# Performance work log

Measured on AMD Instinct MI355X. Metric: run time of the kernel, lower is better.

Reference implementation:

```python
import jax, jax.numpy as jnp
import numpy as np

H = 128

def _gine_conv(x, ei, ea, w1, b1, w2, b2):
    # GINEConv (eps=0): out = MLP(x + sum_{j->i} relu(x_j + e_ji))
    src, dst = ei[0], ei[1]
    m = jax.nn.relu(x[src] + ea)                      # [E, H]
    agg = jax.ops.segment_sum(m, dst, num_segments=x.shape[0])
    h = x + agg
    return jax.nn.relu(h @ w1 + b1) @ w2 + b2

def _bn(x, gamma, beta, eps=1e-5):
    # BatchNorm1d over node dim, batch statistics (training mode)
    mu = jnp.mean(x, axis=0)
    var = jnp.mean((x - mu) ** 2, axis=0)
    return gamma * (x - mu) * jax.lax.rsqrt(var + eps) + beta

def _scatter_mean(vals, ids, mask, n):
    w = mask.astype(vals.dtype)
    s = jax.ops.segment_sum(vals * w[:, None], ids, num_segments=n)
    c = jax.ops.segment_sum(w, ids, num_segments=n)
    return s / jnp.maximum(c, 1.0)[:, None]


def setup_inputs() -> dict:
    key = jax.random.key(0)
    ks = jax.random.split(key, 20)
    Nf, Nt, S, K = 320000, 100000, 20000, 16
    Ei, Eg = 1280000, 800000
    sc = 1.0 / np.sqrt(H)
    inp = {}
    inp["h_flat"] = jax.random.normal(ks[0], (Nf, H), jnp.float32)
    inp["intra_ei"] = jax.random.randint(ks[1], (2, Ei), 0, Nf, jnp.int32)
    inp["ea_flat"] = jax.random.normal(ks[2], (Ei, H), jnp.float32)
    inp["valid"] = jnp.ones((Nf,), jnp.bool_)
    inp["node_ids"] = jax.random.randint(ks[3], (Nf,), 0, Nt, jnp.int32)
    inp["N_total"] = Nt
    inp["edge_index"] = jax.random.randint(ks[4], (2, Eg), 0, Nt, jnp.int32)
    inp["edge_attr"] = jax.random.normal(ks[5], (Eg, H), jnp.float32)
    inp["sub_batch"] = jax.random.randint(ks[6], (Nf,), 0, S, jnp.int32)
    inp["S"] = S
    inp["k"] = K
    inp["root_flat_idx"] = jax.random.randint(ks[7], (S,), 0, Nf, jnp.int32)
    inp["is_root"] = jnp.zeros((Nf,), jnp.bool_)
    # parameters
    inp["local_w1"] = jax.random.normal(ks[8], (H, H), jnp.float32) * sc
    inp["local_b1"] = jnp.zeros((H,), jnp.float32)
    inp["local_w2"] = jax.random.normal(ks[9], (H, H), jnp.float32) * sc
    inp["local_b2"] = jnp.zeros((H,), jnp.float32)
    inp["local_gamma"] = jnp.ones((H,), jnp.float32)
    inp["local_beta"] = jnp.zeros((H,), jnp.float32)
    inp["global_w1"] = jax.random.normal(ks[10], (H, H), jnp.float32) * sc
    inp["global_b1"] = jnp.zeros((H,), jnp.float32)
    inp["global_w2"] = jax.random.normal(ks[11], (H, H), jnp.float32) * sc
    inp["global_b2"] = jnp.zeros((H,), jnp.float32)
    inp["global_gamma"] = jnp.ones((H,), jnp.float32)
    inp["global_beta"] = jnp.zeros((H,), jnp.float32)
    inp["skip_w"] = jax.random.normal(ks[12], (H, H), jnp.float32) * sc
    inp["skip_b"] = jnp.zeros((H,), jnp.float32)
    inp["vv_w"] = jax.random.normal(ks[13], (H, H), jnp.float32) * sc
    inp["vv_b"] = jnp.zeros((H,), jnp.float32)
    inp["kk_w"] = jax.random.normal(ks[14], (H, H), jnp.float32) * sc
    inp["kk_b"] = jnp.zeros((H,), jnp.float32)
    return inp


def reference(h_flat, intra_ei, ea_flat, valid, node_ids, N_total, edge_index, edge_attr,
              sub_batch, S, k, root_flat_idx, is_root,
              local_w1, local_b1, local_w2, local_b2, local_gamma, local_beta,
              global_w1, global_b1, global_w2, global_b2, global_gamma, global_beta,
              skip_w, skip_b, vv_w, vv_b, kk_w, kk_b):
    valid_f = valid.astype(h_flat.dtype)[:, None]
    clamped_ids = jnp.maximum(node_ids, 0)
    valid_mask = node_ids >= 0

    h_skip = (h_flat @ skip_w + skip_b) * valid_f

    h1 = _gine_conv(h_flat, intra_ei, ea_flat, local_w1, local_b1, local_w2, local_b2)
    h1 = _bn(h1, local_gamma, local_beta) * valid_f

    x_sum = _scatter_mean(h_flat, clamped_ids, valid_mask, N_total)   # [N_total, H]
    h2 = _gine_conv(x_sum, edge_index, edge_attr, global_w1, global_b1, global_w2, global_b2)
    h2 = _bn(h2, global_gamma, global_beta)[clamped_ids] * valid_f

    root_ids = node_ids[root_flat_idx]
    root_valid = root_ids >= 0
    x_vv_canonical = _scatter_mean(h_flat[root_flat_idx], jnp.maximum(root_ids, 0), root_valid, N_total)
    x_vv = (x_vv_canonical[clamped_ids] @ vv_w + vv_b) * valid_f

    x_kk = (h_flat[root_flat_idx[sub_batch]] @ kk_w + kk_b) * valid_f

    out = jax.nn.relu(h_skip + h1 + h2 + x_vv + x_kk)
    # dropout p=0.0 -> identity
    return out * valid_f
```

## Files before the change

kernel.cpp:

```cpp
#include <hip/hip_runtime.h>

#define H    128
#define HQ   32
#define TM   64
#define NT   100000
#define XS   136


typedef __attribute__((ext_vector_type(8))) short short8;
typedef __attribute__((ext_vector_type(4))) float f32x4;

static __host__ int cdiv(long a, long b) { return (int)((a + b - 1) / b); }
static __host__ char* alignp(char* p) {
    return (char*)(((uintptr_t)p + 255) & ~(uintptr_t)255);
}

__device__ inline unsigned short f2bf(float f) {
    unsigned u = __float_as_uint(f);
    unsigned r = u + 0x7FFFu + ((u >> 16) & 1u);
    return (unsigned short)(r >> 16);
}
__device__ inline float bf2f(unsigned short u) {
    return __uint_as_float((unsigned)u << 16);
}

__global__ __launch_bounds__(256) void k_cvt(
    const float* __restrict__ in, unsigned short* __restrict__ out, long n8)
{
    long i = (long)blockIdx.x * 256 + threadIdx.x;
    if (i >= n8) return;
    float4 a = ((const float4*)in)[2 * i];
    float4 b = ((const float4*)in)[2 * i + 1];
    ushort4 lo; lo.x = f2bf(a.x); lo.y = f2bf(a.y); lo.z = f2bf(a.z); lo.w = f2bf(a.w);
    ushort4 hi; hi.x = f2bf(b.x); hi.y = f2bf(b.y); hi.z = f2bf(b.z); hi.w = f2bf(b.w);
    ((ushort4*)out)[2 * i]     = lo;
    ((ushort4*)out)[2 * i + 1] = hi;
}

struct CsrJobs {
    const int* ids[4];
    int* cnt[4];
    int* rp[4];
    int* cur[4];
    int* eid[4];
    int  E[4];
    int  N[4];
    int  histBase[5];
    int  scanBase[5];
};

__global__ __launch_bounds__(256) void k_gather_rid(
    const int* __restrict__ node_ids, const int* __restrict__ rfi,
    int* __restrict__ rid, int S)
{
    int i = blockIdx.x * 256 + threadIdx.x;
    if (i >= S) return;
    int nid = node_ids[rfi[i]];
    rid[i] = nid > 0 ? nid : 0;
}

__global__ __launch_bounds__(256) void k_hist4(CsrJobs jb)
{
    int b = blockIdx.x, sg = 0;
    while (b >= jb.histBase[sg + 1]) ++sg;
    int e = (b - jb.histBase[sg]) * 256 + threadIdx.x;
    if (e < jb.E[sg]) atomicAdd(&jb.cnt[sg][jb.ids[sg][e]], 1);
}

__global__ __launch_bounds__(256) void k_scanA4(CsrJobs jb, int* __restrict__ parts)
{
    int b = blockIdx.x, sg = 0;
    while (b >= jb.scanBase[sg + 1]) ++sg;
    int lb = b - jb.scanBase[sg];
    const int* cnt = jb.cnt[sg];
    int* rowptr = jb.rp[sg];
    int N = jb.N[sg];
    int* partials = parts + sg * 256;

    __shared__ int lsum[256];
    int tid = threadIdx.x;
    int base = lb * 2048 + tid * 8;
    int v[8];
    int tsum = 0;
#pragma unroll
    for (int i = 0; i < 8; ++i) {
        int idx = base + i;
        int t = (idx < N) ? cnt[idx] : 0;
        v[i] = tsum;
        tsum += t;
    }
    lsum[tid] = tsum;
    __syncthreads();
    for (int off = 1; off < 256; off <<= 1) {
        int t = (tid >= off) ? lsum[tid - off] : 0;
        __syncthreads();
        lsum[tid] += t;
        __syncthreads();
    }
    int texcl = lsum[tid] - tsum;
#pragma unroll
    for (int i = 0; i < 8; ++i) {
        int idx = base + i;
        if (idx < N) rowptr[idx] = v[i] + texcl;
    }
    if (tid == 255) partials[lb] = lsum[255];
}

__global__ __launch_bounds__(256) void k_scanB4(CsrJobs jb, int* __restrict__ parts)
{
    int sg = blockIdx.x;
    int P = jb.scanBase[sg + 1] - jb.scanBase[sg];
    int* partials = parts + sg * 256;
    int* rowptr = jb.rp[sg];
    int N = jb.N[sg];

    __shared__ int lsum[256];
    int tid = threadIdx.x;
    int val = (tid < P) ? partials[tid] : 0;
    lsum[tid] = val;
    __syncthreads();
    for (int off = 1; off < 256; off <<= 1) {
        int t = (tid >= off) ? lsum[tid - off] : 0;
        __syncthreads();
        lsum[tid] += t;
        __syncthreads();
    }
    if (tid < P) partials[tid] = lsum[tid] - val;
    if (tid == 255) rowptr[N] = lsum[255];
}

__global__ __launch_bounds__(256) void k_scanC4(CsrJobs jb, const int* __restrict__ parts)
{
    int b = blockIdx.x, sg = 0;
    while (b >= jb.scanBase[sg + 1]) ++sg;
    int lb = b - jb.scanBase[sg];
    int off = parts[sg * 256 + lb];
    int N = jb.N[sg];
    int* rowptr = jb.rp[sg];
    int* cursor = jb.cur[sg];
    int base = lb * 2048;
    for (int i = threadIdx.x; i < 2048; i += 256) {
        int g = base + i;
        if (g < N) {
            int v = rowptr[g] + off;
            rowptr[g] = v;
            cursor[g] = v;
        }
    }
}

__global__ __launch_bounds__(256) void k_fillperm4(CsrJobs jb)
{
    int b = blockIdx.x, sg = 0;
    while (b >= jb.histBase[sg + 1]) ++sg;
    int e = (b - jb.histBase[sg]) * 256 + threadIdx.x;
    if (e < jb.E[sg]) {
        int pos = atomicAdd(&jb.cur[sg][jb.ids[sg][e]], 1);
        jb.eid[sg][pos] = e;
    }
}

__global__ __launch_bounds__(256) void k_csr_edge_agg(
    const unsigned short* __restrict__ X, const float* __restrict__ EA,
    const int* __restrict__ src, const int* __restrict__ eid,
    const int* __restrict__ rowptr, unsigned short* __restrict__ OUT, int N)
{
    int idx = blockIdx.x * 256 + threadIdx.x;
    int n = idx >> 5, l = idx & 31;
    if (n >= N) return;
    int beg = rowptr[n], end = rowptr[n + 1];
    float4 acc = {0.f, 0.f, 0.f, 0.f};
    int j = beg;
    for (; j + 2 <= end; j += 2) {
        int e0 = eid[j], e1 = eid[j + 1];
        int s0 = src[e0], s1 = src[e1];
        float4 a0 = ((const float4*)(EA + (size_t)e0 * H))[l];
        ushort4 h0 = ((const ushort4*)(X + (size_t)s0 * H))[l];
        float4 a1 = ((const float4*)(EA + (size_t)e1 * H))[l];
        ushort4 h1 = ((const ushort4*)(X + (size_t)s1 * H))[l];
        acc.x += fmaxf(bf2f(h0.x) + a0.x, 0.f) + fmaxf(bf2f(h1.x) + a1.x, 0.f);
        acc.y += fmaxf(bf2f(h0.y) + a0.y, 0.f) + fmaxf(bf2f(h1.y) + a1.y, 0.f);
        acc.z += fmaxf(bf2f(h0.z) + a0.z, 0.f) + fmaxf(bf2f(h1.z) + a1.z, 0.f);
        acc.w += fmaxf(bf2f(h0.w) + a0.w, 0.f) + fmaxf(bf2f(h1.w) + a1.w, 0.f);
    }
    if (j < end) {
        int e = eid[j];
        int s = src[e];
        float4 a = ((const float4*)(EA + (size_t)e * H))[l];
        ushort4 h = ((const ushort4*)(X + (size_t)s * H))[l];
        acc.x += fmaxf(bf2f(h.x) + a.x, 0.f);
        acc.y += fmaxf(bf2f(h.y) + a.y, 0.f);
        acc.z += fmaxf(bf2f(h.z) + a.z, 0.f);
        acc.w += fmaxf(bf2f(h.w) + a.w, 0.f);
    }
    ushort4 o;
    o.x = f2bf(acc.x); o.y = f2bf(acc.y); o.z = f2bf(acc.z); o.w = f2bf(acc.w);
    ((ushort4*)(OUT + (size_t)n * H))[l] = o;
}

__global__ __launch_bounds__(256) void k_csr_mean(
    const unsigned short* __restrict__ X, const int* __restrict__ eid,
    const int* __restrict__ rowmap,
    const int* __restrict__ rowptr, unsigned short* __restrict__ OUT, int N)
{
    int idx = blockIdx.x * 256 + threadIdx.x;
    int n = idx >> 5, l = idx & 31;
    if (n >= N) return;
    int beg = rowptr[n], end = rowptr[n + 1];
    float4 acc = {0.f, 0.f, 0.f, 0.f};
    int j = beg;
    for (; j + 2 <= end; j += 2) {
        int e0 = eid[j], e1 = eid[j + 1];
        int f0 = rowmap ? rowmap[e0] : e0;
        int f1 = rowmap ? rowmap[e1] : e1;
        ushort4 h0 = ((const ushort4*)(X + (size_t)f0 * H))[l];
        ushort4 h1 = ((const ushort4*)(X + (size_t)f1 * H))[l];
        acc.x += bf2f(h0.x) + bf2f(h1.x); acc.y += bf2f(h0.y) + bf2f(h1.y);
        acc.z += bf2f(h0.z) + bf2f(h1.z); acc.w += bf2f(h0.w) + bf2f(h1.w);
    }
    if (j < end) {
        int e = eid[j];
        int fi = rowmap ? rowmap[e] : e;
        ushort4 h = ((const ushort4*)(X + (size_t)fi * H))[l];
        acc.x += bf2f(h.x); acc.y += bf2f(h.y);
        acc.z += bf2f(h.z); acc.w += bf2f(h.w);
    }
    float inv = 1.0f / fmaxf((float)(end - beg), 1.0f);
    ushort4 o;
    o.x = f2bf(acc.x * inv); o.y = f2bf(acc.y * inv);
    o.z = f2bf(acc.z * inv); o.w = f2bf(acc.w * inv);
    ((ushort4*)(OUT + (size_t)n * H))[l] = o;
}

__device__ inline void stage_x_copy(
    unsigned short* sX, const unsigned short* X1, const int* gidx,
    int r0, int M, int tid)
{
    int r = tid >> 2, q = tid & 3;
    int row = r0 + r;
    unsigned short* dst = &sX[r * XS + q * 32];
    if (row < M) {
        int sr = gidx ? gidx[row] : row;
        const ushort4* xp = (const ushort4*)(X1 + (size_t)sr * H + q * 32);
#pragma unroll
        for (int i = 0; i < 8; ++i) *(ushort4*)(dst + i * 4) = xp[i];
    } else {
#pragma unroll
        for (int i = 0; i < 8; ++i) *(ushort4*)(dst + i * 4) = ushort4{0, 0, 0, 0};
    }
}

__device__ inline void stage_x_sum(
    unsigned short* sX, const unsigned short* X1, const unsigned short* X2,
    int r0, int M, int tid)
{
    int r = tid >> 2, q = tid & 3;
    int row = r0 + r;
    unsigned short* dst = &sX[r * XS + q * 32];
    if (row < M) {
        const ushort4* xp = (const ushort4*)(X1 + (size_t)row * H + q * 32);
        const ushort4* yp = (const ushort4*)(X2 + (size_t)row * H + q * 32);
#pragma unroll
        for (int i = 0; i < 8; ++i) {
            ushort4 a = xp[i], b = yp[i];
            ushort4 o;
            o.x = f2bf(bf2f(a.x) + bf2f(b.x));
            o.y = f2bf(bf2f(a.y) + bf2f(b.y));
            o.z = f2bf(bf2f(a.z) + bf2f(b.z));
            o.w = f2bf(bf2f(a.w) + bf2f(b.w));
            *(ushort4*)(dst + i * 4) = o;
        }
    } else {
#pragma unroll
        for (int i = 0; i < 8; ++i) *(ushort4*)(dst + i * 4) = ushort4{0, 0, 0, 0};
    }
}

__device__ inline void stage_wt(unsigned short* sWT, const float* W, int tid)
{
    for (int f = tid; f < H * HQ; f += 256) {
        int k = f >> 5, n4 = (f & 31) * 4;
        float4 v = ((const float4*)W)[f];
        sWT[(n4 + 0) * XS + k] = f2bf(v.x);
        sWT[(n4 + 1) * XS + k] = f2bf(v.y);
        sWT[(n4 + 2) * XS + k] = f2bf(v.z);
        sWT[(n4 + 3) * XS + k] = f2bf(v.w);
    }
}

__global__ __launch_bounds__(256) void k_gemm(
    const unsigned short* __restrict__ X1, const int* __restrict__ gidx,
    const float* __restrict__ W, const float* __restrict__ B,
    unsigned short* __restrict__ OUT, int M)
{
    __shared__ unsigned short sX[TM * XS];
    __shared__ unsigned short sWT[H * XS];
    __shared__ float sB[H];
    int tid = threadIdx.x;
    int r0 = blockIdx.x * TM;

    stage_x_copy(sX, X1, gidx, r0, M, tid);
    stage_wt(sWT, W, tid);
    if (tid < 32) ((float4*)sB)[tid] = ((const float4*)B)[tid];
    __syncthreads();

    int wv = tid >> 6, l = tid & 63;
    int lr = l & 15, hi = l >> 4, lk = hi * 8;

    f32x4 acc[8];
#pragma unroll
    for (int ct = 0; ct < 8; ++ct) acc[ct] = {0.f, 0.f, 0.f, 0.f};
#pragma unroll
    for (int kk = 0; kk < 4; ++kk) {
        short8 a = *(const short8*)&sX[(wv * 16 + lr) * XS + kk * 32 + lk];
#pragma unroll
        for (int ct = 0; ct < 8; ++ct) {
            short8 b = *(const short8*)&sWT[(ct * 16 + lr) * XS + kk * 32 + lk];
            acc[ct] = __builtin_amdgcn_mfma_f32_16x16x32_bf16(a, b, acc[ct], 0, 0, 0);
        }
    }

    int orow0 = r0 + wv * 16 + hi * 4;
#pragma unroll
    for (int ct = 0; ct < 8; ++ct) {
        int col = ct * 16 + lr;
        float bias = sB[col];
#pragma unroll
        for (int j = 0; j < 4; ++j) {
            int row = orow0 + j;
            if (row >= M) continue;
            OUT[(size_t)row * H + col] = f2bf(acc[ct][j] + bias);
        }
    }
}

__global__ __launch_bounds__(256) void k_mean_gemm(
    const unsigned short* __restrict__ X, const int* __restrict__ eid,
    const int* __restrict__ rowmap, const int* __restrict__ rowptr,
    const float* __restrict__ W, const float* __restrict__ B,
    unsigned short* __restrict__ OUT, int M)
{
    __shared__ unsigned short sX[TM * XS];
    __shared__ unsigned short sWT[H * XS];
    __shared__ float sB[H];
    int tid = threadIdx.x;
    int r0 = blockIdx.x * TM;

    {
        int r = tid >> 2, q = tid & 3;
        int row = r0 + r;
        float4 m[8];
#pragma unroll
        for (int i = 0; i < 8; ++i) m[i] = {0.f, 0.f, 0.f, 0.f};
        int cnt = 0;
        if (row < M) {
            int beg = rowptr[row], end = rowptr[row + 1];
            cnt = end - beg;
            for (int j = beg; j < end; ++j) {
                int fi = rowmap[eid[j]];
                const ushort4* hp = (const ushort4*)(X + (size_t)fi * H + q * 32);
#pragma unroll
                for (int i = 0; i < 8; ++i) {
                    ushort4 v = hp[i];
                    m[i].x += bf2f(v.x); m[i].y += bf2f(v.y);
                    m[i].z += bf2f(v.z); m[i].w += bf2f(v.w);
                }
            }
        }
        float inv = 1.0f / fmaxf((float)cnt, 1.0f);
        unsigned short* dst = &sX[r * XS + q * 32];
#pragma unroll
        for (int i = 0; i < 8; ++i) {
            ushort4 b;
            b.x = f2bf(m[i].x * inv); b.y = f2bf(m[i].y * inv);
            b.z = f2bf(m[i].z * inv); b.w = f2bf(m[i].w * inv);
            *(ushort4*)(dst + i * 4) = b;
        }
    }
    stage_wt(sWT, W, tid);
    if (tid < 32) ((float4*)sB)[tid] = ((const float4*)B)[tid];
    __syncthreads();

    int wv = tid >> 6, l = tid & 63;
    int lr = l & 15, hi = l >> 4, lk = hi * 8;

    f32x4 acc[8];
#pragma unroll
    for (int ct = 0; ct < 8; ++ct) acc[ct] = {0.f, 0.f, 0.f, 0.f};
#pragma unroll
    for (int kk = 0; kk < 4; ++kk) {
        short8 a = *(const short8*)&sX[(wv * 16 + lr) * XS + kk * 32 + lk];
#pragma unroll
        for (int ct = 0; ct < 8; ++ct) {
            short8 b = *(const short8*)&sWT[(ct * 16 + lr) * XS + kk * 32 + lk];
            acc[ct] = __builtin_amdgcn_mfma_f32_16x16x32_bf16(a, b, acc[ct], 0, 0, 0);
        }
    }

    int orow0 = r0 + wv * 16 + hi * 4;
#pragma unroll
    for (int ct = 0; ct < 8; ++ct) {
        int col = ct * 16 + lr;
        float bias = sB[col];
#pragma unroll
        for (int j = 0; j < 4; ++j) {
            int row = orow0 + j;
            if (row >= M) continue;
            OUT[(size_t)row * H + col] = f2bf(acc[ct][j] + bias);
        }
    }
}

__global__ __launch_bounds__(256) void k_mlp(
    const unsigned short* __restrict__ X1, const unsigned short* __restrict__ X2,
    const float* __restrict__ W1, const float* __restrict__ B1,
    const float* __restrict__ W2, const float* __restrict__ B2,
    unsigned short* __restrict__ OUT, int M,
    float* __restrict__ gs, float* __restrict__ gs2)
{
    __shared__ unsigned short sX[TM * XS];
    __shared__ unsigned short sWT[H * XS];
    __shared__ float sB1[H], sB2[H];
    __shared__ float sS[H], sS2[H];
    int tid = threadIdx.x;
    int r0 = blockIdx.x * TM;

    stage_x_sum(sX, X1, X2, r0, M, tid);
    stage_wt(sWT, W1, tid);
    if (tid < 32) ((float4*)sB1)[tid] = ((const float4*)B1)[tid];
    else if (tid < 64) ((float4*)sB2)[tid - 32] = ((const float4*)B2)[tid - 32];
    if (tid >= 64 && tid < 192) { sS[tid - 64] = 0.f; sS2[tid - 64] = 0.f; }
    __syncthreads();

    int wv = tid >> 6, l = tid & 63;
    int lr = l & 15, hi = l >> 4, lk = hi * 8;
    int rloc = wv * 16 + hi * 4;

    f32x4 acc[8];
#pragma unroll
    for (int ct = 0; ct < 8; ++ct) acc[ct] = {0.f, 0.f, 0.f, 0.f};
#pragma unroll
    for (int kk = 0; kk < 4; ++kk) {
        short8 a = *(const short8*)&sX[(wv * 16 + lr) * XS + kk * 32 + lk];
#pragma unroll
        for (int ct = 0; ct < 8; ++ct) {
            short8 b = *(const short8*)&sWT[(ct * 16 + lr) * XS + kk * 32 + lk];
            acc[ct] = __builtin_amdgcn_mfma_f32_16x16x32_bf16(a, b, acc[ct], 0, 0, 0);
        }
    }
    __syncthreads();

#pragma unroll
    for (int ct = 0; ct < 8; ++ct) {
        int c = ct * 16 + lr;
        float b1v = sB1[c];
#pragma unroll
        for (int j = 0; j < 4; ++j) {
            float v = fmaxf(acc[ct][j] + b1v, 0.f);
            int mybf = (int)f2bf(v);
            int other = __shfl_xor(mybf, 1);
            if (!(lr & 1)) {
                unsigned packed = (unsigned)(unsigned short)mybf
                                | ((unsigned)(unsigned short)other << 16);
                *(unsigned*)&sX[(rloc + j) * XS + c] = packed;
            }
        }
        acc[ct] = {0.f, 0.f, 0.f, 0.f};
    }
    stage_wt(sWT, W2, tid);
    __syncthreads();

#pragma unroll
    for (int kk = 0; kk < 4; ++kk) {
        short8 a = *(const short8*)&sX[(wv * 16 + lr) * XS + kk * 32 + lk];
#pragma unroll
        for (int ct = 0; ct < 8; ++ct) {
            short8 b = *(const short8*)&sWT[(ct * 16 + lr) * XS + kk * 32 + lk];
            acc[ct] = __builtin_amdgcn_mfma_f32_16x16x32_bf16(a, b, acc[ct], 0, 0, 0);
        }
    }

    int orow0 = r0 + rloc;
#pragma unroll
    for (int ct = 0; ct < 8; ++ct) {
        int col = ct * 16 + lr;
        float b2v = sB2[col];
        float ps = 0.f, ps2 = 0.f;
#pragma unroll
        for (int j = 0; j < 4; ++j) {
            int row = orow0 + j;
            if (row >= M) continue;
            float o = acc[ct][j] + b2v;
            OUT[(size_t)row * H + col] = f2bf(o);
            ps += o; ps2 += o * o;
        }
        atomicAdd(&sS[col], ps);
        atomicAdd(&sS2[col], ps2);
    }
    __syncthreads();
    if (tid < H) {
        unsafeAtomicAdd(&gs[tid], sS[tid]);
        unsafeAtomicAdd(&gs2[tid], sS2[tid]);
    }
}

__global__ void k_bnfinal(
    const float* __restrict__ s1, const float* __restrict__ s1q,
    const float* __restrict__ g1, const float* __restrict__ be1, float n1,
    const float* __restrict__ s2, const float* __restrict__ s2q,
    const float* __restrict__ g2, const float* __restrict__ be2, float n2,
    float* __restrict__ scale1, float* __restrict__ shift1,
    float* __restrict__ scale2, float* __restrict__ shift2)
{
    int c = threadIdx.x;
    if (c >= H) return;
    float mu = s1[c] / n1;
    float var = s1q[c] / n1 - mu * mu;
    float sc = g1[c] * rsqrtf(var + 1e-5f);
    scale1[c] = sc; shift1[c] = be1[c] - mu * sc;
    mu = s2[c] / n2;
    var = s2q[c] / n2 - mu * mu;
    sc = g2[c] * rsqrtf(var + 1e-5f);
    scale2[c] = sc; shift2[c] = be2[c] - mu * sc;
}

__global__ __launch_bounds__(256) void k_final_gemm(
    const unsigned short* __restrict__ Hf,
    const float* __restrict__ SKW, const float* __restrict__ SKB,
    const unsigned short* __restrict__ h1raw, const unsigned short* __restrict__ h2raw,
    const unsigned short* __restrict__ vvy, const unsigned short* __restrict__ kky,
    const int* __restrict__ node_ids, const int* __restrict__ sub_batch,
    const float* __restrict__ bnp,
    float* __restrict__ OUT, int M)
{
    __shared__ unsigned short sX[TM * XS];
    __shared__ unsigned short sWT[H * XS];
    __shared__ float sP[5 * H];
    int tid = threadIdx.x;
    int r0 = blockIdx.x * TM;

    stage_x_copy(sX, Hf, nullptr, r0, M, tid);
    stage_wt(sWT, SKW, tid);
    if (tid < 160)
        ((float4*)sP)[tid] = (tid < 32) ? ((const float4*)SKB)[tid]
                                        : ((const float4*)bnp)[tid - 32];
    __syncthreads();

    int wv = tid >> 6, l = tid & 63;
    int lr = l & 15, hi = l >> 4, lk = hi * 8;

    f32x4 acc[8];
#pragma unroll
    for (int ct = 0; ct < 8; ++ct) acc[ct] = {0.f, 0.f, 0.f, 0.f};
#pragma unroll
    for (int kk = 0; kk < 4; ++kk) {
        short8 a = *(const short8*)&sX[(wv * 16 + lr) * XS + kk * 32 + lk];
#pragma unroll
        for (int ct = 0; ct < 8; ++ct) {
            short8 b = *(const short8*)&sWT[(ct * 16 + lr) * XS + kk * 32 + lk];
            acc[ct] = __builtin_amdgcn_mfma_f32_16x16x32_bf16(a, b, acc[ct], 0, 0, 0);
        }
    }

    int orow0 = r0 + wv * 16 + hi * 4;
#pragma unroll
    for (int j = 0; j < 4; ++j) {
        int row = orow0 + j;
        if (row >= M) continue;
        int nid = node_ids[row];
        size_t cid = (size_t)(nid > 0 ? nid : 0);
        size_t sb  = (size_t)sub_batch[row];
#pragma unroll
        for (int ct = 0; ct < 8; ++ct) {
            int col = ct * 16 + lr;
            float v = acc[ct][j] + sP[col]
                    + bf2f(h1raw[(size_t)row * H + col]) * sP[H + col] + sP[2 * H + col]
                    + bf2f(h2raw[cid * H + col]) * sP[3 * H + col] + sP[4 * H + col]
                    + bf2f(vvy[cid * H + col]) + bf2f(kky[sb * H + col]);
            OUT[(size_t)row * H + col] = fmaxf(v, 0.f);
        }
    }
}

extern "C" void kernel_launch(void* const* d_in, const int* in_sizes, int n_in,
                              void* d_out, int out_size, void* d_ws, size_t ws_size,
                              hipStream_t stream)
{
    const float* h_flat        = (const float*)d_in[0];
    const int*   intra_ei      = (const int*)d_in[1];
    const float* ea_flat       = (const float*)d_in[2];
    const int*   node_ids      = (const int*)d_in[4];
    const int*   edge_index    = (const int*)d_in[6];
    const float* edge_attr     = (const float*)d_in[7];
    const int*   sub_batch     = (const int*)d_in[8];
    const int*   root_flat_idx = (const int*)d_in[11];
    const float* lw1 = (const float*)d_in[13];
    const float* lb1 = (const float*)d_in[14];
    const float* lw2 = (const float*)d_in[15];
    const float* lb2 = (const float*)d_in[16];
    const float* lg  = (const float*)d_in[17];
    const float* lbe = (const float*)d_in[18];
    const float* gw1 = (const float*)d_in[19];
    const float* gb1 = (const float*)d_in[20];
    const float* gw2 = (const float*)d_in[21];
    const float* gb2 = (const float*)d_in[22];
    const float* gg  = (const float*)d_in[23];
    const float* gbe = (const float*)d_in[24];
    const float* skw = (const float*)d_in[25];
    const float* skb = (const float*)d_in[26];
    const float* vvw = (const float*)d_in[27];
    const float* vvb = (const float*)d_in[28];
    const float* kkw = (const float*)d_in[29];
    const float* kkb = (const float*)d_in[30];

    const int Nf = in_sizes[0] / H;
    const int Ei = in_sizes[2] / H;
    const int Eg = in_sizes[7] / H;
    const int S  = in_sizes[11];

    char* w = (char*)d_ws;
    unsigned short* hbf  = (unsigned short*)w; w += (size_t)Nf * H * 2;
    unsigned short* buf1 = (unsigned short*)w; w += (size_t)Nf * H * 2;
    unsigned short* xsum = (unsigned short*)w; w += (size_t)NT * H * 2;
    unsigned short* buf2 = (unsigned short*)w; w += (size_t)NT * H * 2;
    unsigned short* vvy  = (unsigned short*)w; w += (size_t)NT * H * 2;
    unsigned short* kbuf = (unsigned short*)w; w += (size_t)S * H * 2;
    w = alignp(w);
    float* stats = (float*)w; w += 8 * H * 4;
    w = alignp(w);
    int* cntAll = (int*)w; w += ((size_t)Nf + 3 * (size_t)NT) * 4;
    int* cntA = cntAll;
    int* cntB = cntA + Nf;
    int* cntC = cntB + NT;
    int* cntD = cntC + NT;
    w = alignp(w);
    int* rpA  = (int*)w; w += ((size_t)Nf + 1) * 4;  w = alignp(w);
    int* rpB  = (int*)w; w += ((size_t)NT + 1) * 4;  w = alignp(w);
    int* rpC  = (int*)w; w += ((size_t)NT + 1) * 4;  w = alignp(w);
    int* rpD  = (int*)w; w += ((size_t)NT + 1) * 4;  w = alignp(w);
    int* curA = (int*)w; w += (size_t)Nf * 4;
    int* curB = (int*)w; w += (size_t)NT * 4;
    int* curC = (int*)w; w += (size_t)NT * 4;
    int* curD = (int*)w; w += (size_t)NT * 4;
    int* eidA = (int*)w; w += (size_t)Ei * 4;
    int* eidB = (int*)w; w += (size_t)Eg * 4;
    int* eidC = (int*)w; w += (size_t)Nf * 4;
    int* eidD = (int*)w; w += (size_t)S * 4;
    int* rid  = (int*)w; w += (size_t)S * 4;
    int* parts = (int*)w; w += 4 * 256 * 4;

    k_cvt<<<cdiv((long)Nf * H / 8, 256), 256, 0, stream>>>(
        h_flat, hbf, (long)Nf * H / 8);

    k_gather_rid<<<cdiv(S, 256), 256, 0, stream>>>(node_ids, root_flat_idx, rid, S);

    CsrJobs jb;
    jb.ids[0] = intra_ei + Ei;  jb.ids[1] = edge_index + Eg;
    jb.ids[2] = node_ids;       jb.ids[3] = rid;
    jb.cnt[0] = cntA; jb.cnt[1] = cntB; jb.cnt[2] = cntC; jb.cnt[3] = cntD;
    jb.rp[0]  = rpA;  jb.rp[1]  = rpB;  jb.rp[2]  = rpC;  jb.rp[3]  = rpD;
    jb.cur[0] = curA; jb.cur[1] = curB; jb.cur[2] = curC; jb.cur[3] = curD;
    jb.eid[0] = eidA; jb.eid[1] = eidB; jb.eid[2] = eidC; jb.eid[3] = eidD;
    jb.E[0] = Ei; jb.E[1] = Eg; jb.E[2] = Nf; jb.E[3] = S;
    jb.N[0] = Nf; jb.N[1] = NT; jb.N[2] = NT; jb.N[3] = NT;
    jb.histBase[0] = 0;
    for (int i = 0; i < 4; ++i) jb.histBase[i + 1] = jb.histBase[i] + cdiv(jb.E[i], 256);
    jb.scanBase[0] = 0;
    for (int i = 0; i < 4; ++i) jb.scanBase[i + 1] = jb.scanBase[i] + cdiv(jb.N[i], 2048);

    hipMemsetAsync(cntAll, 0, ((size_t)Nf + 3 * (size_t)NT) * 4, stream);
    k_hist4<<<jb.histBase[4], 256, 0, stream>>>(jb);
    k_scanA4<<<jb.scanBase[4], 256, 0, stream>>>(jb, parts);
    k_scanB4<<<4, 256, 0, stream>>>(jb, parts);
    k_scanC4<<<jb.scanBase[4], 256, 0, stream>>>(jb, parts);
    k_fillperm4<<<jb.histBase[4], 256, 0, stream>>>(jb);

    hipMemsetAsync(stats, 0, 4 * H * 4, stream);

    k_csr_mean<<<cdiv((long)NT * 32, 256), 256, 0, stream>>>(
        hbf, eidC, nullptr, rpC, xsum, NT);
    k_csr_edge_agg<<<cdiv((long)Nf * 32, 256), 256, 0, stream>>>(
        hbf, ea_flat, intra_ei, eidA, rpA, buf1, Nf);
    k_csr_edge_agg<<<cdiv((long)NT * 32, 256), 256, 0, stream>>>(
        xsum, edge_attr, edge_index, eidB, rpB, buf2, NT);

    k_mlp<<<cdiv(Nf, TM), 256, 0, stream>>>(hbf, buf1, lw1, lb1, lw2, lb2,
                                            buf1, Nf, stats, stats + H);
    k_mlp<<<cdiv(NT, TM), 256, 0, stream>>>(xsum, buf2, gw1, gb1, gw2, gb2,
                                            buf2, NT, stats + 2 * H, stats + 3 * H);

    k_mean_gemm<<<cdiv(NT, TM), 256, 0, stream>>>(
        hbf, eidD, root_flat_idx, rpD, vvw, vvb, vvy, NT);
    k_gemm<<<cdiv(S, TM), 256, 0, stream>>>(hbf, root_flat_idx, kkw, kkb,
                                            kbuf, S);

    k_bnfinal<<<1, 128, 0, stream>>>(stats, stats + H, lg, lbe, (float)Nf,
                                     stats + 2 * H, stats + 3 * H, gg, gbe, (float)NT,
                                     stats + 4 * H, stats + 5 * H,
                                     stats + 6 * H, stats + 7 * H);

    k_final_gemm<<<cdiv(Nf, TM), 256, 0, stream>>>(
        hbf, skw, skb, buf1, buf2, vvy, kbuf, node_ids, sub_batch,
        stats + 4 * H, (float*)d_out, Nf);
}
```

Baseline: 1.340 ms.

## Pre-transpose weights once, coalesce final epilogue, fuse small kernels, shuffle-broadcast CSR indices

Adds one kernel that converts and transposes all seven weight matrices to bf16 up front, so each GEMM block does a plain vector copy into shared memory instead of a strided conversion. The CSR aggregation kernels now load 32 edge indices cooperatively and broadcast them with warp shuffles, replacing the serial per-lane index loads. The final GEMM stages its accumulator tile through shared memory so the epilogue reads and writes whole rows coalesced, and it computes the batch-norm scale and shift itself. The root-id gather is folded into the histogram and fill kernels, and the two memsets are merged, which removes several launches at the cost of an extra indirection and more shared-memory traffic.

New measurement: 1.295 ms. 1.03x faster.

```diff
diff --git a/kernel.cpp b/kernel.cpp
--- a/kernel.cpp
+++ b/kernel.cpp
@@ -37,8 +37,24 @@
     ((ushort4*)out)[2 * i + 1] = hi;
 }
 
+struct WJobs { const float* src[7]; };
+
+__global__ __launch_bounds__(256) void k_cvtw(WJobs wj, unsigned short* __restrict__ dstBase)
+{
+    int w = blockIdx.x >> 4, chunk = blockIdx.x & 15;
+    int i = chunk * 256 + threadIdx.x;
+    int k = i >> 5, n4 = (i & 31) * 4;
+    float4 v = ((const float4*)wj.src[w])[i];
+    unsigned short* dst = dstBase + (size_t)w * H * H;
+    dst[(n4 + 0) * H + k] = f2bf(v.x);
+    dst[(n4 + 1) * H + k] = f2bf(v.y);
+    dst[(n4 + 2) * H + k] = f2bf(v.z);
+    dst[(n4 + 3) * H + k] = f2bf(v.w);
+}
+
 struct CsrJobs {
     const int* ids[4];
+    const int* rfi;
     int* cnt[4];
     int* rp[4];
     int* cur[4];
@@ -49,14 +65,13 @@
     int  scanBase[5];
 };
 
-__global__ __launch_bounds__(256) void k_gather_rid(
-    const int* __restrict__ node_ids, const int* __restrict__ rfi,
-    int* __restrict__ rid, int S)
-{
-    int i = blockIdx.x * 256 + threadIdx.x;
-    if (i >= S) return;
-    int nid = node_ids[rfi[i]];
-    rid[i] = nid > 0 ? nid : 0;
+__device__ inline int csr_id(const CsrJobs& jb, int sg, int e)
+{
+    if (sg == 3) {
+        int nid = jb.ids[2][jb.rfi[e]];
+        return nid > 0 ? nid : 0;
+    }
+    return jb.ids[sg][e];
 }
 
 __global__ __launch_bounds__(256) void k_hist4(CsrJobs jb)
@@ -64,7 +79,7 @@
     int b = blockIdx.x, sg = 0;
     while (b >= jb.histBase[sg + 1]) ++sg;
     int e = (b - jb.histBase[sg]) * 256 + threadIdx.x;
-    if (e < jb.E[sg]) atomicAdd(&jb.cnt[sg][jb.ids[sg][e]], 1);
+    if (e < jb.E[sg]) atomicAdd(&jb.cnt[sg][csr_id(jb, sg, e)], 1);
 }
 
 __global__ __launch_bounds__(256) void k_scanA4(CsrJobs jb, int* __restrict__ parts)
@@ -155,7 +170,7 @@
     while (b >= jb.histBase[sg + 1]) ++sg;
     int e = (b - jb.histBase[sg]) * 256 + threadIdx.x;
     if (e < jb.E[sg]) {
-        int pos = atomicAdd(&jb.cur[sg][jb.ids[sg][e]], 1);
+        int pos = atomicAdd(&jb.cur[sg][csr_id(jb, sg, e)], 1);
         jb.eid[sg][pos] = e;
     }
 }
@@ -170,28 +185,20 @@
     if (n >= N) return;
     int beg = rowptr[n], end = rowptr[n + 1];
     float4 acc = {0.f, 0.f, 0.f, 0.f};
-    int j = beg;
-    for (; j + 2 <= end; j += 2) {
-        int e0 = eid[j], e1 = eid[j + 1];
-        int s0 = src[e0], s1 = src[e1];
-        float4 a0 = ((const float4*)(EA + (size_t)e0 * H))[l];
-        ushort4 h0 = ((const ushort4*)(X + (size_t)s0 * H))[l];
-        float4 a1 = ((const float4*)(EA + (size_t)e1 * H))[l];
-        ushort4 h1 = ((const ushort4*)(X + (size_t)s1 * H))[l];
-        acc.x += fmaxf(bf2f(h0.x) + a0.x, 0.f) + fmaxf(bf2f(h1.x) + a1.x, 0.f);
-        acc.y += fmaxf(bf2f(h0.y) + a0.y, 0.f) + fmaxf(bf2f(h1.y) + a1.y, 0.f);
-        acc.z += fmaxf(bf2f(h0.z) + a0.z, 0.f) + fmaxf(bf2f(h1.z) + a1.z, 0.f);
-        acc.w += fmaxf(bf2f(h0.w) + a0.w, 0.f) + fmaxf(bf2f(h1.w) + a1.w, 0.f);
-    }
-    if (j < end) {
-        int e = eid[j];
-        int s = src[e];
-        float4 a = ((const float4*)(EA + (size_t)e * H))[l];
-        ushort4 h = ((const ushort4*)(X + (size_t)s * H))[l];
-        acc.x += fmaxf(bf2f(h.x) + a.x, 0.f);
-        acc.y += fmaxf(bf2f(h.y) + a.y, 0.f);
-        acc.z += fmaxf(bf2f(h.z) + a.z, 0.f);
-        acc.w += fmaxf(bf2f(h.w) + a.w, 0.f);
+    for (int c0 = beg; c0 < end; c0 += 32) {
+        int cnt = min(32, end - c0);
+        int e_l = 0, s_l = 0;
+        if (l < cnt) { e_l = eid[c0 + l]; s_l = src[e_l]; }
+        for (int j = 0; j < cnt; ++j) {
+            int e = __shfl(e_l, j, 32);
+            int s = __shfl(s_l, j, 32);
+            float4 a = ((const float4*)(EA + (size_t)e * H))[l];
+            ushort4 h = ((const ushort4*)(X + (size_t)s * H))[l];
+            acc.x += fmaxf(bf2f(h.x) + a.x, 0.f);
+            acc.y += fmaxf(bf2f(h.y) + a.y, 0.f);
+            acc.z += fmaxf(bf2f(h.z) + a.z, 0.f);
+            acc.w += fmaxf(bf2f(h.w) + a.w, 0.f);
+        }
     }
     ushort4 o;
     o.x = f2bf(acc.x); o.y = f2bf(acc.y); o.z = f2bf(acc.z); o.w = f2bf(acc.w);
@@ -200,7 +207,6 @@
 
 __global__ __launch_bounds__(256) void k_csr_mean(
     const unsigned short* __restrict__ X, const int* __restrict__ eid,
-    const int* __restrict__ rowmap,
     const int* __restrict__ rowptr, unsigned short* __restrict__ OUT, int N)
 {
     int idx = blockIdx.x * 256 + threadIdx.x;
@@ -208,22 +214,16 @@
     if (n >= N) return;
     int beg = rowptr[n], end = rowptr[n + 1];
     float4 acc = {0.f, 0.f, 0.f, 0.f};
-    int j = beg;
-    for (; j + 2 <= end; j += 2) {
-        int e0 = eid[j], e1 = eid[j + 1];
-        int f0 = rowmap ? rowmap[e0] : e0;
-        int f1 = rowmap ? rowmap[e1] : e1;
-        ushort4 h0 = ((const ushort4*)(X + (size_t)f0 * H))[l];
-        ushort4 h1 = ((const ushort4*)(X + (size_t)f1 * H))[l];
-        acc.x += bf2f(h0.x) + bf2f(h1.x); acc.y += bf2f(h0.y) + bf2f(h1.y);
-        acc.z += bf2f(h0.z) + bf2f(h1.z); acc.w += bf2f(h0.w) + bf2f(h1.w);
-    }
-    if (j < end) {
-        int e = eid[j];
-        int fi = rowmap ? rowmap[e] : e;
-        ushort4 h = ((const ushort4*)(X + (size_t)fi * H))[l];
-        acc.x += bf2f(h.x); acc.y += bf2f(h.y);
-        acc.z += bf2f(h.z); acc.w += bf2f(h.w);
+    for (int c0 = beg; c0 < end; c0 += 32) {
+        int cnt = min(32, end - c0);
+        int f_l = 0;
+        if (l < cnt) f_l = eid[c0 + l];
+        for (int j = 0; j < cnt; ++j) {
+            int fi = __shfl(f_l, j, 32);
+            ushort4 h = ((const ushort4*)(X + (size_t)fi * H))[l];
+            acc.x += bf2f(h.x); acc.y += bf2f(h.y);
+            acc.z += bf2f(h.z); acc.w += bf2f(h.w);
+        }
     }
     float inv = 1.0f / fmaxf((float)(end - beg), 1.0f);
     ushort4 o;
@@ -276,21 +276,18 @@
     }
 }
 
-__device__ inline void stage_wt(unsigned short* sWT, const float* W, int tid)
-{
-    for (int f = tid; f < H * HQ; f += 256) {
-        int k = f >> 5, n4 = (f & 31) * 4;
-        float4 v = ((const float4*)W)[f];
-        sWT[(n4 + 0) * XS + k] = f2bf(v.x);
-        sWT[(n4 + 1) * XS + k] = f2bf(v.y);
-        sWT[(n4 + 2) * XS + k] = f2bf(v.z);
-        sWT[(n4 + 3) * XS + k] = f2bf(v.w);
+__device__ inline void stage_wt_pre(
+    unsigned short* sWT, const unsigned short* WT, int tid)
+{
+    for (int i = tid; i < H * HQ; i += 256) {
+        int n = i >> 5, kq = i & 31;
+        *(ushort4*)&sWT[n * XS + kq * 4] = ((const ushort4*)WT)[i];
     }
 }
 
 __global__ __launch_bounds__(256) void k_gemm(
     const unsigned short* __restrict__ X1, const int* __restrict__ gidx,
-    const float* __restrict__ W, const float* __restrict__ B,
+    const unsigned short* __restrict__ WT, const float* __restrict__ B,
     unsigned short* __restrict__ OUT, int M)
 {
     __shared__ unsigned short sX[TM * XS];
@@ -300,7 +297,7 @@
     int r0 = blockIdx.x * TM;
 
     stage_x_copy(sX, X1, gidx, r0, M, tid);
-    stage_wt(sWT, W, tid);
+    stage_wt_pre(sWT, WT, tid);
     if (tid < 32) ((float4*)sB)[tid] = ((const float4*)B)[tid];
     __syncthreads();
 
@@ -337,7 +334,7 @@
 __global__ __launch_bounds__(256) void k_mean_gemm(
     const unsigned short* __restrict__ X, const int* __restrict__ eid,
     const int* __restrict__ rowmap, const int* __restrict__ rowptr,
-    const float* __restrict__ W, const float* __restrict__ B,
+    const unsigned short* __restrict__ WT, const float* __restrict__ B,
     unsigned short* __restrict__ OUT, int M)
 {
     __shared__ unsigned short sX[TM * XS];
@@ -377,7 +374,7 @@
             *(ushort4*)(dst + i * 4) = b;
         }
     }
-    stage_wt(sWT, W, tid);
+    stage_wt_pre(sWT, WT, tid);
     if (tid < 32) ((float4*)sB)[tid] = ((const float4*)B)[tid];
     __syncthreads();
 
@@ -413,8 +410,8 @@
 
 __global__ __launch_bounds__(256) void k_mlp(
     const unsigned short* __restrict__ X1, const unsigned short* __restrict__ X2,
-    const float* __restrict__ W1, const float* __restrict__ B1,
-    const float* __restrict__ W2, const float* __restrict__ B2,
+    const unsigned short* __restrict__ W1T, const float* __restrict__ B1,
+    const unsigned short* __restrict__ W2T, const float* __restrict__ B2,
     unsigned short* __restrict__ OUT, int M,
     float* __restrict__ gs, float* __restrict__ gs2)
 {
@@ -426,7 +423,7 @@
     int r0 = blockIdx.x * TM;
 
     stage_x_sum(sX, X1, X2, r0, M, tid);
-    stage_wt(sWT, W1, tid);
+    stage_wt_pre(sWT, W1T, tid);
     if (tid < 32) ((float4*)sB1)[tid] = ((const float4*)B1)[tid];
     else if (tid < 64) ((float4*)sB2)[tid - 32] = ((const float4*)B2)[tid - 32];
     if (tid >= 64 && tid < 192) { sS[tid - 64] = 0.f; sS2[tid - 64] = 0.f; }
@@ -467,7 +464,7 @@
         }
         acc[ct] = {0.f, 0.f, 0.f, 0.f};
     }
-    stage_wt(sWT, W2, tid);
+    stage_wt_pre(sWT, W2T, tid);
     __syncthreads();
 
 #pragma unroll
@@ -504,33 +501,16 @@
     }
 }
 
-__global__ void k_bnfinal(
-    const float* __restrict__ s1, const float* __restrict__ s1q,
-    const float* __restrict__ g1, const float* __restrict__ be1, float n1,
-    const float* __restrict__ s2, const float* __restrict__ s2q,
-    const float* __restrict__ g2, const float* __restrict__ be2, float n2,
-    float* __restrict__ scale1, float* __restrict__ shift1,
-    float* __restrict__ scale2, float* __restrict__ shift2)
-{
-    int c = threadIdx.x;
-    if (c >= H) return;
-    float mu = s1[c] / n1;
-    float var = s1q[c] / n1 - mu * mu;
-    float sc = g1[c] * rsqrtf(var + 1e-5f);
-    scale1[c] = sc; shift1[c] = be1[c] - mu * sc;
-    mu = s2[c] / n2;
-    var = s2q[c] / n2 - mu * mu;
-    sc = g2[c] * rsqrtf(var + 1e-5f);
-    scale2[c] = sc; shift2[c] = be2[c] - mu * sc;
-}
-
 __global__ __launch_bounds__(256) void k_final_gemm(
     const unsigned short* __restrict__ Hf,
-    const float* __restrict__ SKW, const float* __restrict__ SKB,
+    const unsigned short* __restrict__ SKWT, const float* __restrict__ SKB,
     const unsigned short* __restrict__ h1raw, const unsigned short* __restrict__ h2raw,
     const unsigned short* __restrict__ vvy, const unsigned short* __restrict__ kky,
     const int* __restrict__ node_ids, const int* __restrict__ sub_batch,
-    const float* __restrict__ bnp,
+    const float* __restrict__ stats,
+    const float* __restrict__ lg, const float* __restrict__ lbe,
+    const float* __restrict__ gg, const float* __restrict__ gbe,
+    float n1, float n2,
     float* __restrict__ OUT, int M)
 {
     __shared__ unsigned short sX[TM * XS];
@@ -540,10 +520,19 @@
     int r0 = blockIdx.x * TM;
 
     stage_x_copy(sX, Hf, nullptr, r0, M, tid);
-    stage_wt(sWT, SKW, tid);
-    if (tid < 160)
-        ((float4*)sP)[tid] = (tid < 32) ? ((const float4*)SKB)[tid]
-                                        : ((const float4*)bnp)[tid - 32];
+    stage_wt_pre(sWT, SKWT, tid);
+    if (tid < H) {
+        float mu = stats[tid] / n1;
+        float var = stats[H + tid] / n1 - mu * mu;
+        float sc = lg[tid] * rsqrtf(var + 1e-5f);
+        sP[tid] = sc; sP[H + tid] = lbe[tid] - mu * sc;
+        mu = stats[2 * H + tid] / n2;
+        var = stats[3 * H + tid] / n2 - mu * mu;
+        sc = gg[tid] * rsqrtf(var + 1e-5f);
+        sP[2 * H + tid] = sc; sP[3 * H + tid] = gbe[tid] - mu * sc;
+    } else if (tid < H + 32) {
+        ((float4*)(sP + 4 * H))[tid - H] = ((const float4*)SKB)[tid - H];
+    }
     __syncthreads();
 
     int wv = tid >> 6, l = tid & 63;
@@ -561,23 +550,54 @@
             acc[ct] = __builtin_amdgcn_mfma_f32_16x16x32_bf16(a, b, acc[ct], 0, 0, 0);
         }
     }
-
-    int orow0 = r0 + wv * 16 + hi * 4;
-#pragma unroll
-    for (int j = 0; j < 4; ++j) {
-        int row = orow0 + j;
-        if (row >= M) continue;
-        int nid = node_ids[row];
-        size_t cid = (size_t)(nid > 0 ? nid : 0);
-        size_t sb  = (size_t)sub_batch[row];
-#pragma unroll
-        for (int ct = 0; ct < 8; ++ct) {
-            int col = ct * 16 + lr;
-            float v = acc[ct][j] + sP[col]
-                    + bf2f(h1raw[(size_t)row * H + col]) * sP[H + col] + sP[2 * H + col]
-                    + bf2f(h2raw[cid * H + col]) * sP[3 * H + col] + sP[4 * H + col]
-                    + bf2f(vvy[cid * H + col]) + bf2f(kky[sb * H + col]);
-            OUT[(size_t)row * H + col] = fmaxf(v, 0.f);
+    __syncthreads();
+
+    float* sF = (float*)sWT;
+    int rloc0 = wv * 16 + hi * 4;
+#pragma unroll
+    for (int ct = 0; ct < 8; ++ct) {
+        int col = ct * 16 + lr;
+        float skbv = sP[4 * H + col];
+#pragma unroll
+        for (int j = 0; j < 4; ++j)
+            sF[(rloc0 + j) * 130 + col] = acc[ct][j] + skbv;
+    }
+    __syncthreads();
+
+    {
+        int r = tid >> 2, q = tid & 3;
+        int row = r0 + r;
+        if (row < M) {
+            int nid = node_ids[row];
+            size_t cid = (size_t)(nid > 0 ? nid : 0);
+            size_t sb  = (size_t)sub_batch[row];
+            const ushort4* h1p = (const ushort4*)(h1raw + (size_t)row * H + q * 32);
+            const ushort4* h2p = (const ushort4*)(h2raw + cid * H + q * 32);
+            const ushort4* vvp = (const ushort4*)(vvy + cid * H + q * 32);
+            const ushort4* kkp = (const ushort4*)(kky + sb * H + q * 32);
+            float* op = OUT + (size_t)row * H + q * 32;
+            const float* fr = &sF[r * 130 + q * 32];
+#pragma unroll
+            for (int i = 0; i < 8; ++i) {
+                ushort4 a = h1p[i], b = h2p[i], c = vvp[i], d = kkp[i];
+                int cb = q * 32 + i * 4;
+                float4 o;
+                o.x = fr[i * 4 + 0] + bf2f(a.x) * sP[cb + 0] + sP[H + cb + 0]
+                    + bf2f(b.x) * sP[2 * H + cb + 0] + sP[3 * H + cb + 0]
+                    + bf2f(c.x) + bf2f(d.x);
+                o.y = fr[i * 4 + 1] + bf2f(a.y) * sP[cb + 1] + sP[H + cb + 1]
+                    + bf2f(b.y) * sP[2 * H + cb + 1] + sP[3 * H + cb + 1]
+                    + bf2f(c.y) + bf2f(d.y);
+                o.z = fr[i * 4 + 2] + bf2f(a.z) * sP[cb + 2] + sP[H + cb + 2]
+                    + bf2f(b.z) * sP[2 * H + cb + 2] + sP[3 * H + cb + 2]
+                    + bf2f(c.z) + bf2f(d.z);
+                o.w = fr[i * 4 + 3] + bf2f(a.w) * sP[cb + 3] + sP[H + cb + 3]
+                    + bf2f(b.w) * sP[2 * H + cb + 3] + sP[3 * H + cb + 3]
+                    + bf2f(c.w) + bf2f(d.w);
+                o.x = fmaxf(o.x, 0.f); o.y = fmaxf(o.y, 0.f);
+                o.z = fmaxf(o.z, 0.f); o.w = fmaxf(o.w, 0.f);
+                ((float4*)op)[i] = o;
+            }
         }
     }
 }
@@ -625,14 +645,10 @@
     unsigned short* buf2 = (unsigned short*)w; w += (size_t)NT * H * 2;
     unsigned short* vvy  = (unsigned short*)w; w += (size_t)NT * H * 2;
     unsigned short* kbuf = (unsigned short*)w; w += (size_t)S * H * 2;
-    w = alignp(w);
-    float* stats = (float*)w; w += 8 * H * 4;
+    unsigned short* wtb  = (unsigned short*)w; w += (size_t)7 * H * H * 2;
     w = alignp(w);
     int* cntAll = (int*)w; w += ((size_t)Nf + 3 * (size_t)NT) * 4;
-    int* cntA = cntAll;
-    int* cntB = cntA + Nf;
-    int* cntC = cntB + NT;
-    int* cntD = cntC + NT;
+    float* stats = (float*)w; w += 4 * H * 4;
     w = alignp(w);
     int* rpA  = (int*)w; w += ((size_t)Nf + 1) * 4;  w = alignp(w);
     int* rpB  = (int*)w; w += ((size_t)NT + 1) * 4;  w = alignp(w);
@@ -646,17 +662,25 @@
     int* eidB = (int*)w; w += (size_t)Eg * 4;
     int* eidC = (int*)w; w += (size_t)Nf * 4;
     int* eidD = (int*)w; w += (size_t)S * 4;
-    int* rid  = (int*)w; w += (size_t)S * 4;
     int* parts = (int*)w; w += 4 * 256 * 4;
+    int* cntA = cntAll;
+    int* cntB = cntA + Nf;
+    int* cntC = cntB + NT;
+    int* cntD = cntC + NT;
+
+    hipMemsetAsync(cntAll, 0, ((size_t)Nf + 3 * (size_t)NT) * 4 + 4 * H * 4, stream);
 
     k_cvt<<<cdiv((long)Nf * H / 8, 256), 256, 0, stream>>>(
         h_flat, hbf, (long)Nf * H / 8);
-
-    k_gather_rid<<<cdiv(S, 256), 256, 0, stream>>>(node_ids, root_flat_idx, rid, S);
+    WJobs wj;
+    wj.src[0] = lw1; wj.src[1] = lw2; wj.src[2] = gw1; wj.src[3] = gw2;
+    wj.src[4] = skw; wj.src[5] = vvw; wj.src[6] = kkw;
+    k_cvtw<<<7 * 16, 256, 0, stream>>>(wj, wtb);
 
     CsrJobs jb;
     jb.ids[0] = intra_ei + Ei;  jb.ids[1] = edge_index + Eg;
-    jb.ids[2] = node_ids;       jb.ids[3] = rid;
+    jb.ids[2] = node_ids;       jb.ids[3] = nullptr;
+    jb.rfi = root_flat_idx;
     jb.cnt[0] = cntA; jb.cnt[1] = cntB; jb.cnt[2] = cntC; jb.cnt[3] = cntD;
     jb.rp[0]  = rpA;  jb.rp[1]  = rpB;  jb.rp[2]  = rpC;  jb.rp[3]  = rpD;
     jb.cur[0] = curA; jb.cur[1] = curB; jb.cur[2] = curC; jb.cur[3] = curD;
@@ -668,38 +692,32 @@
     jb.scanBase[0] = 0;
     for (int i = 0; i < 4; ++i) jb.scanBase[i + 1] = jb.scanBase[i] + cdiv(jb.N[i], 2048);
 
-    hipMemsetAsync(cntAll, 0, ((size_t)Nf + 3 * (size_t)NT) * 4, stream);
     k_hist4<<<jb.histBase[4], 256, 0, stream>>>(jb);
     k_scanA4<<<jb.scanBase[4], 256, 0, stream>>>(jb, parts);
     k_scanB4<<<4, 256, 0, stream>>>(jb, parts);
     k_scanC4<<<jb.scanBase[4], 256, 0, stream>>>(jb, parts);
     k_fillperm4<<<jb.histBase[4], 256, 0, stream>>>(jb);
 
-    hipMemsetAsync(stats, 0, 4 * H * 4, stream);
-
     k_csr_mean<<<cdiv((long)NT * 32, 256), 256, 0, stream>>>(
-        hbf, eidC, nullptr, rpC, xsum, NT);
+        hbf, eidC, rpC, xsum, NT);
     k_csr_edge_agg<<<cdiv((long)Nf * 32, 256), 256, 0, stream>>>(
         hbf, ea_flat, intra_ei, eidA, rpA, buf1, Nf);
     k_csr_edge_agg<<<cdiv((long)NT * 32, 256), 256, 0, stream>>>(
         xsum, edge_attr, edge_index, eidB, rpB, buf2, NT);
 
-    k_mlp<<<cdiv(Nf, TM), 256, 0, stream>>>(hbf, buf1, lw1, lb1, lw2, lb2,
+    k_mlp<<<cdiv(Nf, TM), 256, 0, stream>>>(hbf, buf1, wtb + 0 * H * H, lb1,
+                                            wtb + 1 * H * H, lb2,
                                             buf1, Nf, stats, stats + H);
-    k_mlp<<<cdiv(NT, TM), 256, 0, stream>>>(xsum, buf2, gw1, gb1, gw2, gb2,
+    k_mlp<<<cdiv(NT, TM), 256, 0, stream>>>(xsum, buf2, wtb + 2 * H * H, gb1,
+                                            wtb + 3 * H * H, gb2,
                                             buf2, NT, stats + 2 * H, stats + 3 * H);
 
     k_mean_gemm<<<cdiv(NT, TM), 256, 0, stream>>>(
-        hbf, eidD, root_flat_idx, rpD, vvw, vvb, vvy, NT);
-    k_gemm<<<cdiv(S, TM), 256, 0, stream>>>(hbf, root_flat_idx, kkw, kkb,
-                                            kbuf, S);
-
-    k_bnfinal<<<1, 128, 0, stream>>>(stats, stats + H, lg, lbe, (float)Nf,
-                                     stats + 2 * H, stats + 3 * H, gg, gbe, (float)NT,
-                                     stats + 4 * H, stats + 5 * H,
-                                     stats + 6 * H, stats + 7 * H);
+        hbf, eidD, root_flat_idx, rpD, wtb + 5 * H * H, vvb, vvy, NT);
+    k_gemm<<<cdiv(S, TM), 256, 0, stream>>>(hbf, root_flat_idx,
+                                            wtb + 6 * H * H, kkb, kbuf, S);
 
     k_final_gemm<<<cdiv(Nf, TM), 256, 0, stream>>>(
-        hbf, skw, skb, buf1, buf2, vvy, kbuf, node_ids, sub_batch,
-        stats + 4 * H, (float*)d_out, Nf);
-}
+        hbf, wtb + 4 * H * H, skb, buf1, buf2, vvy, kbuf, node_ids, sub_batch,
+        stats, lg, lbe, gg, gbe, (float)Nf, (float)NT, (float*)d_out, Nf);
+}
```
